# Optimization experiments

Hardware: AMD Instinct MI355X
Metric: run time of the kernel (lower is better)

## Reference

```python
import jax, jax.numpy as jnp
import numpy as np

B_SZ, SEQ = 2, 4096
D_MODEL, D_STATE, D_CONV, HEADDIM = 768, 128, 4, 64
D_INNER = 1536
NHEADS = D_INNER // HEADDIM  # 24
D_XBC = D_INNER + 2 * D_STATE  # 1792
D_PROJ = 2 * D_INNER + 2 * D_STATE + NHEADS  # 3352
CHUNK = 128
EPS = 1e-5


def setup_inputs():
    key = jax.random.key(0)
    ks = jax.random.split(key, 10)
    feature = jax.random.normal(ks[0], (B_SZ, SEQ, D_MODEL), jnp.float32)
    in_proj_w = jax.random.normal(ks[1], (D_PROJ, D_MODEL), jnp.float32) * 0.02
    conv_w = jax.random.normal(ks[2], (D_XBC, D_CONV), jnp.float32) * 0.2
    conv_b = jax.random.normal(ks[3], (D_XBC,), jnp.float32) * 0.02
    dt_bias = jnp.log(jnp.expm1(jax.random.uniform(ks[4], (NHEADS,), jnp.float32, 0.001, 0.1)))
    A_log = jnp.log(jax.random.uniform(ks[5], (NHEADS,), jnp.float32, 1.0, 16.0))
    D = jax.random.normal(ks[6], (NHEADS,), jnp.float32) * 0.1 + 1.0
    norm_w = jnp.ones((D_INNER,), jnp.float32)
    out_proj_w = jax.random.normal(ks[7], (D_MODEL, D_INNER), jnp.float32) * 0.02
    gate1 = jnp.float32(0.6)
    return {"feature": feature, "gate1": gate1, "in_proj_w": in_proj_w, "conv_w": conv_w,
            "conv_b": conv_b, "dt_bias": dt_bias, "A_log": A_log, "D": D,
            "norm_w": norm_w, "out_proj_w": out_proj_w}


def segsum(x):
    # x: (..., T) -> (..., T, T); out[..., i, j] = sum_{k=j+1..i} x[..., k]; -inf above diagonal
    T = x.shape[-1]
    xc = jnp.cumsum(x, axis=-1)
    d = xc[..., :, None] - xc[..., None, :]
    mask = jnp.tril(jnp.ones((T, T), bool))
    return jnp.where(mask, d, -jnp.inf)


def ssd(xd, Adt, B, C):
    # Chunked SSD (Mamba2 selective scan). xd: (b,L,H,P) = x*dt; Adt: (b,L,H); B,C: (b,L,N)
    b, L, H, P = xd.shape
    c, Q = L // CHUNK, CHUNK
    xd = xd.reshape(b, c, Q, H, P)
    Adt = Adt.reshape(b, c, Q, H).transpose(0, 3, 1, 2)          # (b,H,c,Q)
    Bc = B.reshape(b, c, Q, -1)
    Cc = C.reshape(b, c, Q, -1)
    A_cum = jnp.cumsum(Adt, axis=-1)                             # (b,H,c,Q)
    Lmat = jnp.exp(segsum(Adt))                                  # (b,H,c,Q,Q)
    CB = jnp.einsum('bcln,bcsn->bcls', Cc, Bc)                   # (b,c,Q,Q)
    Y_diag = jnp.einsum('bcls,bhcls,bcshp->bclhp', CB, Lmat, xd)
    decay_states = jnp.exp(A_cum[..., -1:] - A_cum)              # (b,H,c,Q)
    states = jnp.einsum('bcln,bhcl,bclhp->bchpn', Bc, decay_states, xd)  # (b,c,H,P,N)
    A_last = A_cum[..., -1]                                      # (b,H,c)
    decay_chunk = jnp.exp(segsum(jnp.pad(A_last, ((0, 0), (0, 0), (1, 0)))))  # (b,H,c+1,c+1)
    states_pad = jnp.concatenate([jnp.zeros_like(states[:, :1]), states], axis=1)
    prev = jnp.einsum('bhzc,bchpn->bzhpn', decay_chunk, states_pad)[:, :-1]   # state at chunk start
    Y_off = jnp.einsum('bcln,bhcl,bchpn->bclhp', Cc, jnp.exp(A_cum), prev)
    return (Y_diag + Y_off).reshape(b, L, H, P)


def reference(feature, gate1, in_proj_w, conv_w, conv_b, dt_bias, A_log, D, norm_w, out_proj_w):
    b, L, _ = feature.shape
    zxbcdt = feature @ in_proj_w.T                               # (b,L,3352)
    z = zxbcdt[..., :D_INNER]
    xBC = zxbcdt[..., D_INNER:D_INNER + D_XBC]
    dt = jax.nn.softplus(zxbcdt[..., -NHEADS:] + dt_bias)       # (b,L,H)
    # causal depthwise conv1d (kernel=4) + SiLU
    xp = jnp.pad(xBC, ((0, 0), (D_CONV - 1, 0), (0, 0)))
    xconv = sum(conv_w[:, k] * xp[:, k:k + L, :] for k in range(D_CONV)) + conv_b
    xBC = jax.nn.silu(xconv)
    x = xBC[..., :D_INNER].reshape(b, L, NHEADS, HEADDIM)
    Bm = xBC[..., D_INNER:D_INNER + D_STATE]
    Cm = xBC[..., D_INNER + D_STATE:]
    A = -jnp.exp(A_log)                                          # (H,)
    y = ssd(x * dt[..., None], dt * A, Bm, Cm) + D[:, None] * x  # skip term D*x
    y = y.reshape(b, L, D_INNER)
    # gated RMSNorm (norm_before_gate=False): gate first, then rmsnorm
    y = y * jax.nn.silu(z)
    y = y * jax.lax.rsqrt(jnp.mean(y * y, axis=-1, keepdims=True) + EPS) * norm_w
    out = y @ out_proj_w.T                                       # out_proj (bias=False)
    return jax.nn.sigmoid(gate1) * out + feature
```

## Files before the change

### kernel.cpp

```cpp
#include <hip/hip_runtime.h>
#include <hip/hip_bf16.h>
#include <math.h>

#define B_SZ 2
#define SEQ 4096
#define DMODEL 768
#define DSTATE 128
#define HEADDIM 64
#define DINNER 1536
#define NHEADS 24
#define DXBC 1792
#define DPROJ 3352
#define NPAD1 3456
#define CHUNK 128
#define NCHUNK 32
#define ROWS (B_SZ*SEQ)
#define LDTC 136
#define LDE 136
#define LDE2 132
#define LDEY 65

typedef float floatx4 __attribute__((ext_vector_type(4)));
typedef __bf16 bf16x8 __attribute__((ext_vector_type(8)));

__device__ __forceinline__ float sigmoidf_(float x){ return 1.f/(1.f+__expf(-x)); }
__device__ __forceinline__ float siluf_(float x){ return x/(1.f+__expf(-x)); }
__device__ __forceinline__ float softplusf_(float x){ return (x>20.f)? x : __logf(1.f+__expf(x)); }
__device__ __forceinline__ __bf16 cvt_bf(float x){ __hip_bfloat16 t = __float2bfloat16(x); return *(__bf16*)&t; }

__device__ __forceinline__ void gload_lds16(const __hip_bfloat16* g, __hip_bfloat16* l){
    __builtin_amdgcn_global_load_lds(
        (const __attribute__((address_space(1))) void*)g,
        (__attribute__((address_space(3))) void*)l, 16, 0, 0);
}

__global__ __launch_bounds__(512)
void gemm1_mfma(const __hip_bfloat16* __restrict__ A,
                const __hip_bfloat16* __restrict__ W,
                __hip_bfloat16* __restrict__ z16, __hip_bfloat16* __restrict__ xbc16,
                float* __restrict__ dtb, const float* __restrict__ dt_bias)
{
    __shared__ __align__(16) char smem[49152];
    __hip_bfloat16* Asm = (__hip_bfloat16*)smem;
    __hip_bfloat16* Wsm = Asm + 256*64;
    const int tid = threadIdx.x;
    const int lane = tid & 63, wave = tid >> 6;
    const int blk = blockIdx.x;
    const int m_tile = ((blk & 7) << 2) | ((blk >> 3) & 3);
    const int bx = blk >> 5;
    const int bm = m_tile*256, bn = bx*128;
    const int wm = (wave & 3)*64, wn = (wave >> 2)*64;
    const int r16 = lane & 15, qbase = lane >> 4, sw = r16 & 7;
    floatx4 acc[4][4] = {};
    for (int k0 = 0; k0 < DMODEL; k0 += 64) {
#pragma unroll
        for (int j = 0; j < 4; ++j) {
            int cc = j*512 + tid;
            int row = cc >> 3, jc = cc & 7;
            int sj = jc ^ (row & 7);
            gload_lds16(A + (size_t)(bm+row)*DMODEL + k0 + sj*8, Asm + cc*8);
        }
#pragma unroll
        for (int j = 0; j < 2; ++j) {
            int cc = j*512 + tid;
            int row = cc >> 3, jc = cc & 7;
            int sj = jc ^ (row & 7);
            gload_lds16(W + (size_t)(bn+row)*DMODEL + k0 + sj*8, Wsm + cc*8);
        }
        __syncthreads();
#pragma unroll
        for (int ks = 0; ks < 2; ++ks) {
            const int kq = ((qbase + ks*4) ^ sw)*8;
            bf16x8 af[4], wf[4];
#pragma unroll
            for (int i = 0; i < 4; ++i) {
                af[i] = *(const bf16x8*)(Asm + (wm + i*16 + r16)*64 + kq);
                wf[i] = *(const bf16x8*)(Wsm + (wn + i*16 + r16)*64 + kq);
            }
#pragma unroll
            for (int mi = 0; mi < 4; ++mi)
#pragma unroll
                for (int ni = 0; ni < 4; ++ni)
                    acc[mi][ni] = __builtin_amdgcn_mfma_f32_16x16x32_bf16(
                        af[mi], wf[ni], acc[mi][ni], 0, 0, 0);
        }
        __syncthreads();
    }
    const int col = lane & 15, rowq = (lane >> 4)*4;
    if (bx == 26) {
        if (wn == 0) {
#pragma unroll
            for (int mi = 0; mi < 4; ++mi)
#pragma unroll
                for (int ni = 0; ni < 2; ++ni) {
                    int h = ni*16 + col;
                    if (h < NHEADS)
#pragma unroll
                        for (int r = 0; r < 4; ++r) {
                            int m = bm + wm + mi*16 + rowq + r;
                            dtb[(size_t)m*NHEADS + h] =
                                softplusf_(acc[mi][ni][r] + dt_bias[h]);
                        }
                }
        }
        return;
    }
    __hip_bfloat16* Tsm = (__hip_bfloat16*)smem;
    __hip_bfloat16* dst; int ldd;
    if (bx < 12) { dst = z16 + bn;            ldd = DINNER; }
    else         { dst = xbc16 + bn - DINNER; ldd = DXBC;  }
    for (int half = 0; half < 2; ++half) {
        if (((wave & 3) >> 1) == half) {
#pragma unroll
            for (int mi = 0; mi < 4; ++mi)
#pragma unroll
                for (int ni = 0; ni < 4; ++ni)
#pragma unroll
                    for (int r = 0; r < 4; ++r)
                        Tsm[(wm - half*128 + mi*16 + rowq + r)*LDE + wn + ni*16 + col] =
                            __float2bfloat16(acc[mi][ni][r]);
        }
        __syncthreads();
#pragma unroll
        for (int it = 0; it < 4; ++it) {
            int e = it*512 + tid;
            int row = e >> 4, c0 = (e & 15)*8;
            bf16x8 v = *(const bf16x8*)(Tsm + row*LDE + c0);
            *(bf16x8*)(dst + (size_t)(bm + half*128 + row)*ldd + c0) = v;
        }
        __syncthreads();
    }
}

__global__ __launch_bounds__(256)
void gemm2_mfma(const __hip_bfloat16* __restrict__ A,
                const __hip_bfloat16* __restrict__ W,
                float* __restrict__ C,
                const float* __restrict__ gate, const float* __restrict__ resid,
                const float* __restrict__ rowsq)
{
    __shared__ __align__(16) char smem[33792];
    __shared__ float scale_lds[128];
    __hip_bfloat16* Asm = (__hip_bfloat16*)smem;
    __hip_bfloat16* Wsm = Asm + 128*64;
    const int tid = threadIdx.x;
    const int lane = tid & 63, wave = tid >> 6;
    const int blk = blockIdx.x;
    const int mblk = blk & 63;
    const int m_tile = ((mblk & 7) << 3) | (mblk >> 3);
    const int bm = m_tile*128, bn = (blk >> 6)*128;
    const int wm = (wave & 1)*64, wn = (wave >> 1)*64;
    const int r16 = lane & 15, qbase = lane >> 4, sw = r16 & 7;
    floatx4 acc[4][4] = {};
    for (int k0 = 0; k0 < DINNER; k0 += 64) {
#pragma unroll
        for (int j = 0; j < 4; ++j) {
            int cc = j*256 + tid;
            int row = cc >> 3, jc = cc & 7;
            int sj = jc ^ (row & 7);
            gload_lds16(A + (size_t)(bm+row)*DINNER + k0 + sj*8, Asm + cc*8);
        }
#pragma unroll
        for (int j = 0; j < 4; ++j) {
            int cc = j*256 + tid;
            int row = cc >> 3, jc = cc & 7;
            int sj = jc ^ (row & 7);
            gload_lds16(W + (size_t)(bn+row)*DINNER + k0 + sj*8, Wsm + cc*8);
        }
        __syncthreads();
#pragma unroll
        for (int ks = 0; ks < 2; ++ks) {
            const int kq = ((qbase + ks*4) ^ sw)*8;
            bf16x8 af[4], wf[4];
#pragma unroll
            for (int i = 0; i < 4; ++i) {
                af[i] = *(const bf16x8*)(Asm + (wm + i*16 + r16)*64 + kq);
                wf[i] = *(const bf16x8*)(Wsm + (wn + i*16 + r16)*64 + kq);
            }
#pragma unroll
            for (int mi = 0; mi < 4; ++mi)
#pragma unroll
                for (int ni = 0; ni < 4; ++ni)
                    acc[mi][ni] = __builtin_amdgcn_mfma_f32_16x16x32_bf16(
                        af[mi], wf[ni], acc[mi][ni], 0, 0, 0);
        }
        __syncthreads();
    }
    if (tid < 128)
        scale_lds[tid] = rsqrtf(rowsq[bm + tid] * (1.f/DINNER) + 1e-5f);
    float gs = sigmoidf_(gate[0]);
    __syncthreads();
    const int col = lane & 15, rowq = (lane >> 4)*4;
    float* Tsm = (float*)smem;
    for (int half = 0; half < 2; ++half) {
        if ((wave & 1) == half) {
#pragma unroll
            for (int mi = 0; mi < 4; ++mi)
#pragma unroll
                for (int ni = 0; ni < 4; ++ni)
#pragma unroll
                    for (int r = 0; r < 4; ++r)
                        Tsm[(mi*16 + rowq + r)*LDE2 + wn + ni*16 + col] = acc[mi][ni][r];
        }
        __syncthreads();
#pragma unroll
        for (int it = 0; it < 8; ++it) {
            int e = it*256 + tid;
            int row = e >> 5, c0 = (e & 31)*4;
            float4 v = *(const float4*)(Tsm + row*LDE2 + c0);
            float sc = gs * scale_lds[half*64 + row];
            size_t off = (size_t)(bm + half*64 + row)*DMODEL + bn + c0;
            float4 rv = *(const float4*)(resid + off);
            v.x = sc*v.x + rv.x; v.y = sc*v.y + rv.y;
            v.z = sc*v.z + rv.z; v.w = sc*v.w + rv.w;
            *(float4*)(C + off) = v;
        }
        __syncthreads();
    }
}

#define NC1 (ROWS*DMODEL)
#define NC2 (NPAD1*DMODEL)
#define NC3 (DMODEL*DINNER)
#define NV1 (NC1/8)
#define NV2 (NC2/8)
#define NV3 (NC3/8)
__global__ __launch_bounds__(256)
void cast_all(const float* __restrict__ feature, const float* __restrict__ in_w,
              const float* __restrict__ out_w, const float* __restrict__ nw,
              __hip_bfloat16* __restrict__ fbf, __hip_bfloat16* __restrict__ wbf,
              __hip_bfloat16* __restrict__ owbf)
{
    int v = blockIdx.x*256 + threadIdx.x;
    if (v < NV1) {
        int i = v*8;
        float4 a = *(const float4*)(feature + i);
        float4 b = *(const float4*)(feature + i + 4);
        bf16x8 o;
        o[0]=cvt_bf(a.x); o[1]=cvt_bf(a.y); o[2]=cvt_bf(a.z); o[3]=cvt_bf(a.w);
        o[4]=cvt_bf(b.x); o[5]=cvt_bf(b.y); o[6]=cvt_bf(b.z); o[7]=cvt_bf(b.w);
        *(bf16x8*)(fbf + i) = o;
    } else if (v < NV1 + NV2) {
        int j = (v - NV1)*8;
        int n = j / DMODEL, k = j - n*DMODEL;
        bf16x8 o;
        if (n < DPROJ) {
            const float* s = in_w + (size_t)n*DMODEL + k;
            float4 a = *(const float4*)(s);
            float4 b = *(const float4*)(s + 4);
            o[0]=cvt_bf(a.x); o[1]=cvt_bf(a.y); o[2]=cvt_bf(a.z); o[3]=cvt_bf(a.w);
            o[4]=cvt_bf(b.x); o[5]=cvt_bf(b.y); o[6]=cvt_bf(b.z); o[7]=cvt_bf(b.w);
        } else {
#pragma unroll
            for (int q = 0; q < 8; ++q) o[q] = (__bf16)0.f;
        }
        *(bf16x8*)(wbf + j) = o;
    } else if (v < NV1 + NV2 + NV3) {
        int j = (v - NV1 - NV2)*8;
        int k = j % DINNER;
        float4 a  = *(const float4*)(out_w + j);
        float4 b  = *(const float4*)(out_w + j + 4);
        float4 na = *(const float4*)(nw + k);
        float4 nb = *(const float4*)(nw + k + 4);
        bf16x8 o;
        o[0]=cvt_bf(a.x*na.x); o[1]=cvt_bf(a.y*na.y); o[2]=cvt_bf(a.z*na.z); o[3]=cvt_bf(a.w*na.w);
        o[4]=cvt_bf(b.x*nb.x); o[5]=cvt_bf(b.y*nb.y); o[6]=cvt_bf(b.z*nb.z); o[7]=cvt_bf(b.w*nb.w);
        *(bf16x8*)(owbf + j) = o;
    }
}

__global__ __launch_bounds__(256)
void conv_scan_k(const __hip_bfloat16* __restrict__ xbc16, const float* __restrict__ cw,
                 const float* __restrict__ cbias,
                 __hip_bfloat16* __restrict__ x_t,
                 __hip_bfloat16* __restrict__ B_n, __hip_bfloat16* __restrict__ B_t,
                 __hip_bfloat16* __restrict__ C_n,
                 const float* __restrict__ dtb, const float* __restrict__ A_log,
                 float* __restrict__ acum)
{
    int xb = blockIdx.x;
    if (xb >= 14) {
        __shared__ float sh2[256];
        int h = xb - 14, c = blockIdx.y, b = blockIdx.z;
        int tid = threadIdx.x;
        int l = tid & 127, g2 = tid >> 7;
        float* sh = sh2 + g2*128;
        float Aa = -__expf(A_log[h]);
        size_t row = (size_t)b*SEQ + c*CHUNK + l;
        float v = dtb[row*NHEADS + h] * Aa;
        sh[l] = v; __syncthreads();
        for (int off=1; off<128; off<<=1){
            float t = (l>=off) ? sh[l-off] : 0.f;
            __syncthreads();
            sh[l] += t;
            __syncthreads();
        }
        if (g2 == 0)
            acum[((b*NHEADS+h)*NCHUNK + c)*CHUNK + l] = sh[l];
        return;
    }
    __shared__ __align__(16) __hip_bfloat16 in[131*LDTC];
    int ct = xb, lt = blockIdx.y, b = blockIdx.z;
    int tid = threadIdx.x;
    int base = lt*128;
    for (int it = 0; it < 2096; it += 256) {
        int e = it + tid; if (e >= 2096) break;
        int row = e >> 4, c0 = (e & 15)*8;
        int l = base - 3 + row;
        bf16x8 v;
        if (l < 0) { for (int j = 0; j < 8; ++j) v[j] = (__bf16)0.f; }
        else v = *(const bf16x8*)(xbc16 + ((size_t)b*SEQ + l)*DXBC + ct*128 + c0);
        *(bf16x8*)(in + row*LDTC + c0) = v;
    }
    __syncthreads();
    int ch = tid & 127, lh = tid >> 7, l0 = lh*64;
    int g = ct*128 + ch;
    float w0 = cw[g*4+0], w1 = cw[g*4+1], w2 = cw[g*4+2], w3 = cw[g*4+3];
    float bias = cbias[g];
    float a0 = __bfloat162float(in[(l0+0)*LDTC + ch]);
    float a1 = __bfloat162float(in[(l0+1)*LDTC + ch]);
    float a2 = __bfloat162float(in[(l0+2)*LDTC + ch]);
    size_t trow = 0;
    if (ct < 12)      trow = ((size_t)b*NHEADS + (g>>6))*HEADDIM + (g & 63);
    else if (ct == 12) trow = (size_t)b*DSTATE + ch;
    bf16x8 obuf;
#pragma unroll
    for (int li = 0; li < 64; ++li) {
        float a3 = __bfloat162float(in[(l0+li+3)*LDTC + ch]);
        float o = siluf_(bias + w0*a0 + w1*a1 + w2*a2 + w3*a3);
        a0 = a1; a1 = a2; a2 = a3;
        __hip_bfloat16 ob = __float2bfloat16(o);
        size_t rr = (size_t)b*SEQ + base + l0 + li;
        if (ct == 12)      B_n[rr*DSTATE + ch] = ob;
        else if (ct == 13) C_n[rr*DSTATE + ch] = ob;
        obuf[li & 7] = *(const __bf16*)&ob;
        if ((li & 7) == 7 && ct <= 12) {
            __hip_bfloat16* dst = (ct < 12) ? x_t : B_t;
            *(bf16x8*)(dst + trow*SEQ + base + l0 + (li - 7)) = obuf;
        }
    }
}

__global__ __launch_bounds__(256)
void cbst_k(const __hip_bfloat16* __restrict__ B_n, const __hip_bfloat16* __restrict__ C_n,
            __hip_bfloat16* __restrict__ CB16,
            const __hip_bfloat16* __restrict__ x_t, const __hip_bfloat16* __restrict__ B_t,
            const float* __restrict__ dtb, const float* __restrict__ acum,
            __hip_bfloat16* __restrict__ states)
{
    int bid = blockIdx.x;
    int tid = threadIdx.x, lane = tid & 63, wave = tid >> 6;
    if (bid < 64) {
        int c = bid & 31, b = bid >> 5;
        size_t base = (size_t)b*SEQ + c*CHUNK;
        int r16 = lane & 15, kq = (lane>>4)*8;
        floatx4 acc[2][8] = {};
#pragma unroll
        for (int ks = 0; ks < 4; ++ks) {
            int k0 = ks*32 + kq;
            bf16x8 af[2], bfv[8];
#pragma unroll
            for (int mt = 0; mt < 2; ++mt)
                af[mt] = *(const bf16x8*)(C_n + (base + (wave*2+mt)*16 + r16)*DSTATE + k0);
#pragma unroll
            for (int st = 0; st < 8; ++st)
                bfv[st] = *(const bf16x8*)(B_n + (base + st*16 + r16)*DSTATE + k0);
#pragma unroll
            for (int mt = 0; mt < 2; ++mt)
#pragma unroll
                for (int st = 0; st < 8; ++st)
                    if (st <= wave*2+mt)
                        acc[mt][st] = __builtin_amdgcn_mfma_f32_16x16x32_bf16(
                            af[mt], bfv[st], acc[mt][st], 0,0,0);
        }
        size_t cbb = (size_t)(b*NCHUNK+c)*CHUNK*CHUNK;
        int scol = lane & 15, rowq = (lane>>4)*4;
#pragma unroll
        for (int mt = 0; mt < 2; ++mt)
#pragma unroll
            for (int st = 0; st < 8; ++st)
                if (st <= wave*2+mt)
#pragma unroll
                    for (int r = 0; r < 4; ++r)
                        CB16[cbb + (size_t)((wave*2+mt)*16 + rowq + r)*CHUNK + st*16 + scol] =
                            __float2bfloat16(acc[mt][st][r]);
        return;
    }
    __shared__ float f[128];
    int t = bid - 64;
    int c = t & 31;
    int h = (t>>5) % NHEADS;
    int b = t/(32*NHEADS);
    int arow = ((b*NHEADS+h)*NCHUNK + c)*CHUNK;
    size_t rbase = (size_t)b*SEQ + c*CHUNK;
    if (tid < 128) {
        float alast = acum[arow + 127];
        f[tid] = dtb[(rbase + tid)*NHEADS + h] * __expf(alast - acum[arow + tid]);
    }
    __syncthreads();
    int r16 = lane & 15, kq = (lane>>4)*8;
    size_t xtb = ((size_t)b*NHEADS + h)*HEADDIM;
    int cl = c*CHUNK;
    floatx4 acc[8] = {};
#pragma unroll
    for (int ks = 0; ks < 4; ++ks) {
        int k0 = ks*32 + kq;
        bf16x8 xa = *(const bf16x8*)(x_t + (xtb + wave*16 + r16)*SEQ + cl + k0);
        bf16x8 af;
#pragma unroll
        for (int j = 0; j < 8; ++j)
            af[j] = (__bf16)((float)xa[j] * f[k0 + j]);
        bf16x8 bfv[8];
#pragma unroll
        for (int nt = 0; nt < 8; ++nt)
            bfv[nt] = *(const bf16x8*)(B_t + ((size_t)b*DSTATE + nt*16 + r16)*SEQ + cl + k0);
#pragma unroll
        for (int nt = 0; nt < 8; ++nt)
            acc[nt] = __builtin_amdgcn_mfma_f32_16x16x32_bf16(af, bfv[nt], acc[nt], 0,0,0);
    }
    size_t sb = ((size_t)(b*NCHUNK+c)*NHEADS + h)*(HEADDIM*DSTATE);
    int ncol = lane & 15, rowq = (lane>>4)*4;
#pragma unroll
    for (int nt = 0; nt < 8; ++nt)
#pragma unroll
        for (int r = 0; r < 4; ++r)
            states[sb + (size_t)(wave*16 + rowq + r)*DSTATE + nt*16 + ncol] =
                __float2bfloat16(acc[nt][r]);
}

__global__ __launch_bounds__(64)
void recur_k(__hip_bfloat16* __restrict__ states, const float* __restrict__ acum)
{
    int pb = blockIdx.x & 15;
    int bh = blockIdx.x >> 4;
    int h = bh % NHEADS, b = bh / NHEADS;
    int voff = (pb*64 + threadIdx.x)*8;
    const size_t cstride = (size_t)NHEADS*HEADDIM*DSTATE;
    size_t base0 = ((size_t)(b*NCHUNK)*NHEADS + h)*(HEADDIM*DSTATE) + voff;
    bf16x8 st[NCHUNK];
    float ev[NCHUNK];
#pragma unroll
    for (int c = 0; c < NCHUNK; ++c)
        st[c] = *(const bf16x8*)(states + base0 + (size_t)c*cstride);
#pragma unroll
    for (int c = 0; c < NCHUNK; ++c)
        ev[c] = __expf(acum[((b*NHEADS+h)*NCHUNK + c)*CHUNK + 127]);
    float S[8] = {};
#pragma unroll
    for (int c = 0; c < NCHUNK; ++c) {
        bf16x8 pv;
#pragma unroll
        for (int j = 0; j < 8; ++j) {
            pv[j] = (__bf16)S[j];
            S[j] = S[j]*ev[c] + (float)st[c][j];
        }
        *(bf16x8*)(states + base0 + (size_t)c*cstride) = pv;
    }
}

__global__ __launch_bounds__(512, 4)
void y_mfma(const __hip_bfloat16* __restrict__ x_t, const __hip_bfloat16* __restrict__ z16,
            const __hip_bfloat16* __restrict__ C_n, const __hip_bfloat16* __restrict__ CB16,
            const __hip_bfloat16* __restrict__ states, const float* __restrict__ dtb,
            const float* __restrict__ acum, const float* __restrict__ Dp,
            __hip_bfloat16* __restrict__ y16, float* __restrict__ rowsq)
{
    __shared__ __align__(16) char smem[33280];
    __hip_bfloat16* XT = (__hip_bfloat16*)smem;
    __hip_bfloat16* ST = XT + 64*128;
    float* Tsm = (float*)smem;
    __shared__ float ac[128], dts[128], gk[128];
    const int tid = threadIdx.x, lane = tid & 63, wave = tid >> 6;
    const int r16 = lane & 15, kq = (lane>>4)*8;
    const int l = wave*16 + r16;
    const int pcol = lane & 15, rowq = (lane>>4)*4;
    const int erow = tid >> 2, ec0 = (tid & 3)*16;
#pragma unroll 1
    for (int u = blockIdx.x; u < B_SZ*NHEADS*NCHUNK; u += 512) {
        int c = u & 31;
        int h = (u>>5) % NHEADS;
        int b = u/(32*NHEADS);
        int arow = ((b*NHEADS+h)*NCHUNK + c)*CHUNK;
        size_t rbase = (size_t)b*SEQ + c*CHUNK;
        size_t xtb = ((size_t)b*NHEADS + h)*HEADDIM;
        size_t sb  = ((size_t)(b*NCHUNK+c)*NHEADS + h)*(HEADDIM*DSTATE);
        size_t cbb = (size_t)(b*NCHUNK+c)*CHUNK*CHUNK;
        int cl = c*CHUNK;
#pragma unroll
        for (int j = 0; j < 2; ++j) {
            int cc = j*512 + tid;
            int p = cc >> 4, ch = cc & 15;
            int sj = ch ^ (p & 7);
            gload_lds16(x_t + (xtb + p)*SEQ + cl + sj*8, XT + cc*8);
            gload_lds16(states + sb + (size_t)p*DSTATE + sj*8, ST + cc*8);
        }
        if (tid < 128) {
            ac[tid]  = acum[arow + tid];
            dts[tid] = dtb[(rbase + tid)*NHEADS + h];
        }
        __syncthreads();
        if (tid < 128)
            gk[tid] = __expf(ac[tid & 96] - ac[tid]) * dts[tid];
        bf16x8 cb[4], cv[4];
#pragma unroll
        for (int ks = 0; ks < 4; ++ks) {
            cb[ks] = *(const bf16x8*)(CB16 + cbb + (size_t)l*CHUNK + ks*32 + kq);
            cv[ks] = *(const bf16x8*)(C_n + (rbase + l)*DSTATE + ks*32 + kq);
        }
        bf16x8 zA = *(const bf16x8*)(z16 + (rbase + erow)*DINNER + h*HEADDIM + ec0);
        bf16x8 zB = *(const bf16x8*)(z16 + (rbase + erow)*DINNER + h*HEADDIM + ec0 + 8);
        __syncthreads();
        float acl = ac[l];
        float Dh = Dp[h];
        floatx4 acc[4] = {};
        int nks = (wave >> 1) + 1;
#pragma unroll
        for (int ks = 0; ks < 4; ++ks) {
            if (ks < nks) {
                int k0 = ks*32 + kq;
                float fl = __expf(acl - ac[ks*32]);
                bf16x8 af;
#pragma unroll
                for (int j = 0; j < 8; ++j) {
                    int s = k0 + j;
                    float w = (s <= l) ? (float)cb[ks][j] * (fl * gk[s]) : 0.f;
                    if (s == l) w += Dh;
                    af[j] = (__bf16)w;
                }
                int chL = k0 >> 3;
                bf16x8 bfv[4];
#pragma unroll
                for (int pt = 0; pt < 4; ++pt) {
                    int row = pt*16 + r16;
                    bfv[pt] = *(const bf16x8*)(XT + (row*16 + (chL ^ (row & 7)))*8);
                }
#pragma unroll
                for (int pt = 0; pt < 4; ++pt)
                    acc[pt] = __builtin_amdgcn_mfma_f32_16x16x32_bf16(af, bfv[pt], acc[pt], 0,0,0);
            }
        }
        float eal = __expf(acl);
#pragma unroll
        for (int ks = 0; ks < 4; ++ks) {
            int k0 = ks*32 + kq;
            bf16x8 af;
#pragma unroll
            for (int j = 0; j < 8; ++j)
                af[j] = (__bf16)((float)cv[ks][j] * eal);
            int chL = k0 >> 3;
            bf16x8 bfv[4];
#pragma unroll
            for (int pt = 0; pt < 4; ++pt) {
                int row = pt*16 + r16;
                bfv[pt] = *(const bf16x8*)(ST + (row*16 + (chL ^ (row & 7)))*8);
            }
#pragma unroll
            for (int pt = 0; pt < 4; ++pt)
                acc[pt] = __builtin_amdgcn_mfma_f32_16x16x32_bf16(af, bfv[pt], acc[pt], 0,0,0);
        }
        __syncthreads();
#pragma unroll
        for (int pt = 0; pt < 4; ++pt)
#pragma unroll
            for (int r = 0; r < 4; ++r)
                Tsm[(wave*16 + rowq + r)*LDEY + pt*16 + pcol] = acc[pt][r];
        __syncthreads();
        {
            float s = 0.f; bf16x8 o1, o2;
#pragma unroll
            for (int j2 = 0; j2 < 8; ++j2) {
                float g = Tsm[erow*LDEY + ec0 + j2] * siluf_(__bfloat162float(zA[j2]));
                o1[j2] = cvt_bf(g); s += g*g;
            }
#pragma unroll
            for (int j2 = 0; j2 < 8; ++j2) {
                float g = Tsm[erow*LDEY + ec0 + 8 + j2] * siluf_(__bfloat162float(zB[j2]));
                o2[j2] = cvt_bf(g); s += g*g;
            }
            size_t grow = rbase + erow;
            *(bf16x8*)(y16 + grow*DINNER + h*HEADDIM + ec0)     = o1;
            *(bf16x8*)(y16 + grow*DINNER + h*HEADDIM + ec0 + 8) = o2;
            s += __shfl_xor(s, 1); s += __shfl_xor(s, 2);
            if ((tid & 3) == 0)
                atomicAdd(rowsq + grow, s);
        }
        __syncthreads();
    }
}

extern "C" void kernel_launch(void* const* d_in, const int* in_sizes, int n_in,
                              void* d_out, int out_size, void* d_ws, size_t ws_size,
                              hipStream_t stream)
{
    const float* feature = (const float*)d_in[0];
    const float* gate1   = (const float*)d_in[1];
    const float* in_w    = (const float*)d_in[2];
    const float* conv_w  = (const float*)d_in[3];
    const float* conv_b  = (const float*)d_in[4];
    const float* dt_bias = (const float*)d_in[5];
    const float* A_log   = (const float*)d_in[6];
    const float* Dp      = (const float*)d_in[7];
    const float* norm_w  = (const float*)d_in[8];
    const float* out_w   = (const float*)d_in[9];
    float* out = (float*)d_out;

    char* p = (char*)d_ws;
    __hip_bfloat16* z16   = (__hip_bfloat16*)p; p += (size_t)ROWS*DINNER*2;
    __hip_bfloat16* xbc16 = (__hip_bfloat16*)p; p += (size_t)ROWS*DXBC*2;
    __hip_bfloat16* x_t   = (__hip_bfloat16*)p; p += (size_t)ROWS*DINNER*2;
    __hip_bfloat16* B_n   = (__hip_bfloat16*)p; p += (size_t)ROWS*DSTATE*2;
    __hip_bfloat16* B_t   = (__hip_bfloat16*)p; p += (size_t)ROWS*DSTATE*2;
    __hip_bfloat16* C_n   = (__hip_bfloat16*)p; p += (size_t)ROWS*DSTATE*2;
    float* dtb    = (float*)p;            p += (size_t)ROWS*NHEADS*4;
    float* acum   = (float*)p;            p += (size_t)B_SZ*NHEADS*NCHUNK*CHUNK*4;
    float* rowsq  = (float*)p;            p += (size_t)ROWS*4;
    __hip_bfloat16* CB16 = (__hip_bfloat16*)p; p += (size_t)B_SZ*NCHUNK*CHUNK*CHUNK*2;
    __hip_bfloat16* states = (__hip_bfloat16*)p; p += (size_t)B_SZ*NCHUNK*NHEADS*HEADDIM*DSTATE*2;
    __hip_bfloat16* y16  = (__hip_bfloat16*)p; p += (size_t)ROWS*DINNER*2;
    __hip_bfloat16* fbf  = (__hip_bfloat16*)p; p += (size_t)ROWS*DMODEL*2;
    __hip_bfloat16* wbf  = (__hip_bfloat16*)p; p += (size_t)NPAD1*DMODEL*2;
    __hip_bfloat16* owbf = (__hip_bfloat16*)p; p += (size_t)DMODEL*DINNER*2;

    cast_all<<<(NV1+NV2+NV3+255)/256, 256, 0, stream>>>(feature, in_w, out_w, norm_w,
                                                        fbf, wbf, owbf);
    hipMemsetAsync(rowsq, 0, (size_t)ROWS*4, stream);

    gemm1_mfma<<<27*32, 512, 0, stream>>>(fbf, wbf, z16, xbc16, dtb, dt_bias);
    conv_scan_k<<<dim3(14 + NHEADS, 32, B_SZ), 256, 0, stream>>>(
        xbc16, conv_w, conv_b, x_t, B_n, B_t, C_n, dtb, A_log, acum);
    cbst_k<<<64 + B_SZ*NHEADS*NCHUNK, 256, 0, stream>>>(
        B_n, C_n, CB16, x_t, B_t, dtb, acum, states);
    recur_k<<<B_SZ*NHEADS*16, 64, 0, stream>>>(states, acum);
    y_mfma<<<512, 512, 0, stream>>>(x_t, z16, C_n, CB16, states,
                                    dtb, acum, Dp, y16, rowsq);
    gemm2_mfma<<<6*64, 256, 0, stream>>>(y16, owbf, out, gate1, feature, rowsq);
}
```

Baseline: 286.0 us.

## Prefetch next y tile, fold rowsq memset into cast, shuffle-scan cumsum

```diff
diff --git a/kernel.cpp b/kernel.cpp
--- a/kernel.cpp
+++ b/kernel.cpp
@@ -225,11 +225,12 @@
 #define NV1 (NC1/8)
 #define NV2 (NC2/8)
 #define NV3 (NC3/8)
+#define NVR (ROWS/8)
 __global__ __launch_bounds__(256)
 void cast_all(const float* __restrict__ feature, const float* __restrict__ in_w,
               const float* __restrict__ out_w, const float* __restrict__ nw,
               __hip_bfloat16* __restrict__ fbf, __hip_bfloat16* __restrict__ wbf,
-              __hip_bfloat16* __restrict__ owbf)
+              __hip_bfloat16* __restrict__ owbf, float* __restrict__ rowsq)
 {
     int v = blockIdx.x*256 + threadIdx.x;
     if (v < NV1) {
@@ -266,10 +267,15 @@
         o[0]=cvt_bf(a.x*na.x); o[1]=cvt_bf(a.y*na.y); o[2]=cvt_bf(a.z*na.z); o[3]=cvt_bf(a.w*na.w);
         o[4]=cvt_bf(b.x*nb.x); o[5]=cvt_bf(b.y*nb.y); o[6]=cvt_bf(b.z*nb.z); o[7]=cvt_bf(b.w*nb.w);
         *(bf16x8*)(owbf + j) = o;
-    }
-}
-
-__global__ __launch_bounds__(256)
+    } else if (v < NV1 + NV2 + NV3 + NVR) {
+        int j = (v - NV1 - NV2 - NV3)*8;
+        float4 z = {0.f, 0.f, 0.f, 0.f};
+        *(float4*)(rowsq + j) = z;
+        *(float4*)(rowsq + j + 4) = z;
+    }
+}
+
+__global__ __launch_bounds__(512)
 void conv_scan_k(const __hip_bfloat16* __restrict__ xbc16, const float* __restrict__ cw,
                  const float* __restrict__ cbias,
                  __hip_bfloat16* __restrict__ x_t,
@@ -279,31 +285,32 @@
                  float* __restrict__ acum)
 {
     int xb = blockIdx.x;
+    int tid = threadIdx.x;
     if (xb >= 14) {
-        __shared__ float sh2[256];
+        __shared__ float wtot;
         int h = xb - 14, c = blockIdx.y, b = blockIdx.z;
-        int tid = threadIdx.x;
-        int l = tid & 127, g2 = tid >> 7;
-        float* sh = sh2 + g2*128;
-        float Aa = -__expf(A_log[h]);
-        size_t row = (size_t)b*SEQ + c*CHUNK + l;
-        float v = dtb[row*NHEADS + h] * Aa;
-        sh[l] = v; __syncthreads();
-        for (int off=1; off<128; off<<=1){
-            float t = (l>=off) ? sh[l-off] : 0.f;
-            __syncthreads();
-            sh[l] += t;
-            __syncthreads();
-        }
-        if (g2 == 0)
-            acum[((b*NHEADS+h)*NCHUNK + c)*CHUNK + l] = sh[l];
+        int lane = tid & 63;
+        float s = 0.f;
+        if (tid < 128) {
+            float Aa = -__expf(A_log[h]);
+            s = dtb[((size_t)b*SEQ + c*CHUNK + tid)*NHEADS + h] * Aa;
+#pragma unroll
+            for (int off = 1; off < 64; off <<= 1) {
+                float t = __shfl_up(s, off);
+                if (lane >= off) s += t;
+            }
+            if (tid == 63) wtot = s;
+        }
+        __syncthreads();
+        if (tid >= 64 && tid < 128) s += wtot;
+        if (tid < 128)
+            acum[((b*NHEADS+h)*NCHUNK + c)*CHUNK + tid] = s;
         return;
     }
     __shared__ __align__(16) __hip_bfloat16 in[131*LDTC];
     int ct = xb, lt = blockIdx.y, b = blockIdx.z;
-    int tid = threadIdx.x;
     int base = lt*128;
-    for (int it = 0; it < 2096; it += 256) {
+    for (int it = 0; it < 2096; it += 512) {
         int e = it + tid; if (e >= 2096) break;
         int row = e >> 4, c0 = (e & 15)*8;
         int l = base - 3 + row;
@@ -313,7 +320,7 @@
         *(bf16x8*)(in + row*LDTC + c0) = v;
     }
     __syncthreads();
-    int ch = tid & 127, lh = tid >> 7, l0 = lh*64;
+    int ch = tid & 127, lh = tid >> 7, l0 = lh*32;
     int g = ct*128 + ch;
     float w0 = cw[g*4+0], w1 = cw[g*4+1], w2 = cw[g*4+2], w3 = cw[g*4+3];
     float bias = cbias[g];
@@ -325,7 +332,7 @@
     else if (ct == 12) trow = (size_t)b*DSTATE + ch;
     bf16x8 obuf;
 #pragma unroll
-    for (int li = 0; li < 64; ++li) {
+    for (int li = 0; li < 32; ++li) {
         float a3 = __bfloat162float(in[(l0+li+3)*LDTC + ch]);
         float o = siluf_(bias + w0*a0 + w1*a1 + w2*a2 + w3*a3);
         a0 = a1; a1 = a2; a2 = a3;
@@ -465,26 +472,22 @@
             const float* __restrict__ acum, const float* __restrict__ Dp,
             __hip_bfloat16* __restrict__ y16, float* __restrict__ rowsq)
 {
-    __shared__ __align__(16) char smem[33280];
+    __shared__ __align__(16) char smem[32768];
     __hip_bfloat16* XT = (__hip_bfloat16*)smem;
     __hip_bfloat16* ST = XT + 64*128;
-    float* Tsm = (float*)smem;
+    __shared__ __align__(16) float Tsm[128*LDEY];
     __shared__ float ac[128], dts[128], gk[128];
     const int tid = threadIdx.x, lane = tid & 63, wave = tid >> 6;
     const int r16 = lane & 15, kq = (lane>>4)*8;
     const int l = wave*16 + r16;
     const int pcol = lane & 15, rowq = (lane>>4)*4;
     const int erow = tid >> 2, ec0 = (tid & 3)*16;
-#pragma unroll 1
-    for (int u = blockIdx.x; u < B_SZ*NHEADS*NCHUNK; u += 512) {
-        int c = u & 31;
-        int h = (u>>5) % NHEADS;
-        int b = u/(32*NHEADS);
-        int arow = ((b*NHEADS+h)*NCHUNK + c)*CHUNK;
-        size_t rbase = (size_t)b*SEQ + c*CHUNK;
+    const int NU = B_SZ*NHEADS*NCHUNK;
+    {
+        int u = blockIdx.x;
+        int c = u & 31, h = (u>>5) % NHEADS, b = u/(32*NHEADS);
         size_t xtb = ((size_t)b*NHEADS + h)*HEADDIM;
         size_t sb  = ((size_t)(b*NCHUNK+c)*NHEADS + h)*(HEADDIM*DSTATE);
-        size_t cbb = (size_t)(b*NCHUNK+c)*CHUNK*CHUNK;
         int cl = c*CHUNK;
 #pragma unroll
         for (int j = 0; j < 2; ++j) {
@@ -494,6 +497,15 @@
             gload_lds16(x_t + (xtb + p)*SEQ + cl + sj*8, XT + cc*8);
             gload_lds16(states + sb + (size_t)p*DSTATE + sj*8, ST + cc*8);
         }
+    }
+#pragma unroll 1
+    for (int u = blockIdx.x; u < NU; u += 512) {
+        int c = u & 31;
+        int h = (u>>5) % NHEADS;
+        int b = u/(32*NHEADS);
+        int arow = ((b*NHEADS+h)*NCHUNK + c)*CHUNK;
+        size_t rbase = (size_t)b*SEQ + c*CHUNK;
+        size_t cbb = (size_t)(b*NCHUNK+c)*CHUNK*CHUNK;
         if (tid < 128) {
             ac[tid]  = acum[arow + tid];
             dts[tid] = dtb[(rbase + tid)*NHEADS + h];
@@ -559,6 +571,21 @@
                 acc[pt] = __builtin_amdgcn_mfma_f32_16x16x32_bf16(af, bfv[pt], acc[pt], 0,0,0);
         }
         __syncthreads();
+        int un = u + 512;
+        if (un < NU) {
+            int c2 = un & 31, h2 = (un>>5) % NHEADS, b2 = un/(32*NHEADS);
+            size_t xtb2 = ((size_t)b2*NHEADS + h2)*HEADDIM;
+            size_t sb2  = ((size_t)(b2*NCHUNK+c2)*NHEADS + h2)*(HEADDIM*DSTATE);
+            int cl2 = c2*CHUNK;
+#pragma unroll
+            for (int j = 0; j < 2; ++j) {
+                int cc = j*512 + tid;
+                int p = cc >> 4, ch = cc & 15;
+                int sj = ch ^ (p & 7);
+                gload_lds16(x_t + (xtb2 + p)*SEQ + cl2 + sj*8, XT + cc*8);
+                gload_lds16(states + sb2 + (size_t)p*DSTATE + sj*8, ST + cc*8);
+            }
+        }
 #pragma unroll
         for (int pt = 0; pt < 4; ++pt)
 #pragma unroll
@@ -584,7 +611,6 @@
             if ((tid & 3) == 0)
                 atomicAdd(rowsq + grow, s);
         }
-        __syncthreads();
     }
 }
 
@@ -621,12 +647,11 @@
     __hip_bfloat16* wbf  = (__hip_bfloat16*)p; p += (size_t)NPAD1*DMODEL*2;
     __hip_bfloat16* owbf = (__hip_bfloat16*)p; p += (size_t)DMODEL*DINNER*2;
 
-    cast_all<<<(NV1+NV2+NV3+255)/256, 256, 0, stream>>>(feature, in_w, out_w, norm_w,
-                                                        fbf, wbf, owbf);
-    hipMemsetAsync(rowsq, 0, (size_t)ROWS*4, stream);
+    cast_all<<<(NV1+NV2+NV3+NVR+255)/256, 256, 0, stream>>>(feature, in_w, out_w, norm_w,
+                                                            fbf, wbf, owbf, rowsq);
 
     gemm1_mfma<<<27*32, 512, 0, stream>>>(fbf, wbf, z16, xbc16, dtb, dt_bias);
-    conv_scan_k<<<dim3(14 + NHEADS, 32, B_SZ), 256, 0, stream>>>(
+    conv_scan_k<<<dim3(14 + NHEADS, 32, B_SZ), 512, 0, stream>>>(
         xbc16, conv_w, conv_b, x_t, B_n, B_t, C_n, dtb, A_log, acum);
     cbst_k<<<64 + B_SZ*NHEADS*NCHUNK, 256, 0, stream>>>(
         B_n, C_n, CB16, x_t, B_t, dtb, acum, states);
```

Result: faster. 277.4 us (-3.0%).
